# Kernel optimization log

Measured on AMD Instinct MI355X. Metric: run time of the kernel, lower is better.

## Reference

```python
import jax, jax.numpy as jnp
import numpy as np

ITEMNUM = 50000
NUM_HEADS = 4
EPS = 1e-8


def _ln(x, g, b):
    m = x.mean(-1, keepdims=True)
    v = ((x - m) ** 2).mean(-1, keepdims=True)
    return (x - m) * jax.lax.rsqrt(v + EPS) * g + b


def _forward(seqs_data, position, seqs, time_emb, pos_table, gate_W, gate_b,
             ln_attn_g, ln_attn_b, qW, qb, kW, kb, vW, vb,
             ln_ffn_g, ln_ffn_b, c1W, c1b, c2W, c2b, last_g, last_b):
    B, L, H = seqs.shape
    nb = qW.shape[0]
    hd = H // NUM_HEADS

    pe = pos_table[position]                      # [B,L,H]
    seqs = seqs + pe
    time = time_emb + pe
    # per-position per-block time gates, [B,L,nb]
    gates = jax.nn.sigmoid(jnp.einsum('blh,nh->bln', time, gate_W) + gate_b)

    keep = (seqs_data != ITEMNUM - 1)[..., None].astype(seqs.dtype)  # [B,L,1]
    seqs = seqs * keep
    tril = jnp.tril(jnp.ones((L, L), dtype=bool))  # causal: keep lower triangle
    neg_inf = jnp.asarray(-jnp.inf, seqs.dtype)
    scale = 1.0 / np.sqrt(hd).astype(np.float32)

    for i in range(nb):
        Q = _ln(seqs, ln_attn_g[i], ln_attn_b[i])
        q = Q @ qW[i].T + qb[i]
        k = time @ kW[i].T + kb[i]
        v = (seqs + time) @ vW[i].T + vb[i]
        # [B,nh,L,hd]
        q = q.reshape(B, L, NUM_HEADS, hd).transpose(0, 2, 1, 3)
        k = k.reshape(B, L, NUM_HEADS, hd).transpose(0, 2, 1, 3)
        v = v.reshape(B, L, NUM_HEADS, hd).transpose(0, 2, 1, 3)
        scores = jnp.einsum('bhqd,bhkd->bhqk', q, k) * scale  # [B,nh,L,L]
        tg = gates[:, :, i]                                   # [B,L]
        gate_mat = tg[:, None, :, None] * tg[:, None, None, :]  # [B,1,L,L] outer product
        scores = jnp.where(tril[None, None], scores * gate_mat, neg_inf)
        attn = jax.nn.softmax(scores, axis=-1)
        out = jnp.einsum('bhqk,bhkd->bhqd', attn, v)
        out = out.transpose(0, 2, 1, 3).reshape(B, L, H)
        x = Q + out
        x = _ln(x, ln_ffn_g[i], ln_ffn_b[i])
        # PointWiseFeedForward: two 1x1 convs == two linears, relu, residual
        h = jax.nn.relu(x @ c1W[i].T + c1b[i])
        seqs = (h @ c2W[i].T + c2b[i] + x) * keep

    return _ln(seqs, last_g, last_b)


def setup_inputs() -> dict:
    key = jax.random.key(0)
    B, L, H, NB, ML = 64, 512, 256, 2, 512
    ks = iter(jax.random.split(key, 32))
    nrm = lambda shape, s=0.05: jax.random.normal(next(ks), shape, jnp.float32) * s
    pos_table = nrm((ML, H), 0.02).at[0].set(0.0)  # padding_idx=0
    inp = {
        'seqs_data': jax.random.randint(next(ks), (B, L), 0, ITEMNUM - 1, jnp.int32),
        'seqs': nrm((B, L, H), 1.0),
        'position': jax.random.randint(next(ks), (B, L), 0, ML, jnp.int32),
        'time_emb': nrm((B, L, H), 1.0),
        'pos_table': pos_table,
        'gate_W': nrm((NB, H)), 'gate_b': jnp.zeros((NB,), jnp.float32),
        'ln_attn_g': jnp.ones((NB, H), jnp.float32), 'ln_attn_b': jnp.zeros((NB, H), jnp.float32),
        'qW': nrm((NB, H, H)), 'qb': jnp.zeros((NB, H), jnp.float32),
        'kW': nrm((NB, H, H)), 'kb': jnp.zeros((NB, H), jnp.float32),
        'vW': nrm((NB, H, H)), 'vb': jnp.zeros((NB, H), jnp.float32),
        'ln_ffn_g': jnp.ones((NB, H), jnp.float32), 'ln_ffn_b': jnp.zeros((NB, H), jnp.float32),
        'c1W': nrm((NB, H, H)), 'c1b': jnp.zeros((NB, H), jnp.float32),
        'c2W': nrm((NB, H, H)), 'c2b': jnp.zeros((NB, H), jnp.float32),
        'last_g': jnp.ones((H,), jnp.float32), 'last_b': jnp.zeros((H,), jnp.float32),
    }
    return inp


def reference(seqs_data, seqs, position, time_emb, pos_table, gate_W, gate_b,
              ln_attn_g, ln_attn_b, qW, qb, kW, kb, vW, vb,
              ln_ffn_g, ln_ffn_b, c1W, c1b, c2W, c2b, last_g, last_b):
    return _forward(seqs_data, position, seqs, time_emb, pos_table, gate_W, gate_b,
                    ln_attn_g, ln_attn_b, qW, qb, kW, kb, vW, vb,
                    ln_ffn_g, ln_ffn_b, c1W, c1b, c2W, c2b, last_g, last_b)
```

## Files before the change

kernel.cpp:

```cpp
#include <hip/hip_runtime.h>
#include <hip/hip_bf16.h>
#include <math.h>

#define NTOK 32768
#define Hdim 256
#define Ldim 512
#define Bdim 64
#define NHEAD 4
#define HD 64
#define PADV 49999

typedef __bf16 bf16x8 __attribute__((ext_vector_type(8)));
typedef __bf16 bf16x4 __attribute__((ext_vector_type(4)));
typedef float  f32x4  __attribute__((ext_vector_type(4)));
typedef unsigned short u16x8 __attribute__((ext_vector_type(8)));

union bf8u { bf16x8 v8; bf16x4 v4[2]; };

__device__ __forceinline__ unsigned short f2bf(float f) {
    unsigned int u = __float_as_uint(f);
    unsigned int r = (u + 0x7fffu + ((u >> 16) & 1u)) >> 16;
    return (unsigned short)r;
}
__device__ __forceinline__ float bf2f(unsigned short u) {
    return __uint_as_float(((unsigned int)u) << 16);
}

__device__ __forceinline__ void gload16(const void* g, void* l) {
    __builtin_amdgcn_global_load_lds((const __attribute__((address_space(1))) unsigned int*)g,
                                     (__attribute__((address_space(3))) unsigned int*)l,
                                     16, 0, 0);
}

__global__ __launch_bounds__(256)
void castw_kernel(const float* __restrict__ q, const float* __restrict__ k,
                  const float* __restrict__ v, const float* __restrict__ c1,
                  const float* __restrict__ c2, unsigned short* __restrict__ dst) {
    const float* srcs[5] = {q, k, v, c1, c2};
    const float* s = srcs[blockIdx.y];
    int idx = blockIdx.x * 1024 + threadIdx.x * 4;
    float4 f = *(const float4*)(s + idx);
    unsigned short* d = dst + (size_t)blockIdx.y * 131072 + idx;
    d[0] = f2bf(f.x); d[1] = f2bf(f.y); d[2] = f2bf(f.z); d[3] = f2bf(f.w);
}

__global__ __launch_bounds__(256)
void prep_ln_kernel(const int* __restrict__ seqs_data, const float* __restrict__ seqs,
                    const int* __restrict__ position, const float* __restrict__ time_emb,
                    const float* __restrict__ pos_table, const float* __restrict__ gate_W,
                    const float* __restrict__ gate_b,
                    const float* __restrict__ lnG, const float* __restrict__ lnB,
                    unsigned short* __restrict__ Tbf,
                    unsigned short* __restrict__ QXbf,
                    unsigned short* __restrict__ VINbf,
                    float* __restrict__ gates, float* __restrict__ keepv) {
    int tok  = blockIdx.x * 4 + (threadIdx.x >> 6);
    int lane = threadIdx.x & 63;
    size_t off = (size_t)tok * Hdim + lane * 4;
    int pos = position[tok];
    float4 pe = *(const float4*)(pos_table + (size_t)pos * Hdim + lane * 4);
    float4 sq = *(const float4*)(seqs + off);
    float4 tm = *(const float4*)(time_emb + off);
    float keep = (seqs_data[tok] != PADV) ? 1.0f : 0.0f;
    float4 t = {tm.x + pe.x, tm.y + pe.y, tm.z + pe.z, tm.w + pe.w};
    float4 s = {(sq.x + pe.x) * keep, (sq.y + pe.y) * keep,
                (sq.z + pe.z) * keep, (sq.w + pe.w) * keep};
    ushort4 tb = {f2bf(t.x), f2bf(t.y), f2bf(t.z), f2bf(t.w)};
    *(ushort4*)(Tbf + off) = tb;
    float4 gw0 = *(const float4*)(gate_W + lane * 4);
    float4 gw1 = *(const float4*)(gate_W + Hdim + lane * 4);
    float r0 = s.x + s.y + s.z + s.w;
    float r1 = s.x * s.x + s.y * s.y + s.z * s.z + s.w * s.w;
    float r2 = t.x * gw0.x + t.y * gw0.y + t.z * gw0.z + t.w * gw0.w;
    float r3 = t.x * gw1.x + t.y * gw1.y + t.z * gw1.z + t.w * gw1.w;
#pragma unroll
    for (int o = 1; o < 64; o <<= 1) {
        r0 += __shfl_xor(r0, o, 64);
        r1 += __shfl_xor(r1, o, 64);
        r2 += __shfl_xor(r2, o, 64);
        r3 += __shfl_xor(r3, o, 64);
    }
    float mean = r0 * (1.0f / Hdim);
    float var  = fmaxf(r1 * (1.0f / Hdim) - mean * mean, 0.0f);
    float rstd = rsqrtf(var + 1e-8f);
    if (lane == 0) {
        gates[(size_t)tok * 2 + 0] = 1.0f / (1.0f + __expf(-(r2 + gate_b[0])));
        gates[(size_t)tok * 2 + 1] = 1.0f / (1.0f + __expf(-(r3 + gate_b[1])));
        keepv[tok] = keep;
    }
    float4 g4 = *(const float4*)(lnG + lane * 4);
    float4 b4 = *(const float4*)(lnB + lane * 4);
    float4 y = {(s.x - mean) * rstd * g4.x + b4.x, (s.y - mean) * rstd * g4.y + b4.y,
                (s.z - mean) * rstd * g4.z + b4.z, (s.w - mean) * rstd * g4.w + b4.w};
    ushort4 yb = {f2bf(y.x), f2bf(y.y), f2bf(y.z), f2bf(y.w)};
    *(ushort4*)(QXbf + off) = yb;
    ushort4 vb = {f2bf(s.x + t.x), f2bf(s.y + t.y), f2bf(s.z + t.z), f2bf(s.w + t.w)};
    *(ushort4*)(VINbf + off) = vb;
}

#define GBM 128
#define GBN 128
#define GBK 64

__device__ __forceinline__ void stage64(const unsigned short* __restrict__ src,
                                        size_t rowBase, __bf16* lds, int tid, int kc) {
#pragma unroll
    for (int it = 0; it < 4; ++it) {
        int c = tid + it * 256;
        int r = c >> 3, sub = c & 7;
        int g = sub ^ (r & 7);
        gload16(src + (rowBase + r) * Hdim + kc + g * 8, lds + c * 8);
    }
}
__device__ __forceinline__ bf16x8 frag64(const __bf16* lds, int r, int g) {
    return *(const bf16x8*)(lds + r * 64 + (g ^ (r & 7)) * 8);
}

__global__ __launch_bounds__(256)
void gemm_qkv_kernel(const unsigned short* __restrict__ QXbf,
                     const unsigned short* __restrict__ Tbf,
                     const unsigned short* __restrict__ VINbf,
                     const unsigned short* __restrict__ qW,
                     const unsigned short* __restrict__ kW,
                     const unsigned short* __restrict__ vW,
                     const float* __restrict__ qb, const float* __restrict__ kb,
                     const float* __restrict__ vb,
                     unsigned short* __restrict__ Qbf,
                     unsigned short* __restrict__ Kbf,
                     unsigned short* __restrict__ VT) {
    __shared__ __align__(16) char smem[128 * 136 * 2];
    __bf16* As = (__bf16*)smem;
    __bf16* Ws = (__bf16*)(smem + 16384);
    __bf16 (*Ct)[136] = (__bf16 (*)[136])smem;
    int z = blockIdx.z;
    const unsigned short* A = (z == 0) ? QXbf : (z == 1) ? Tbf : VINbf;
    const unsigned short* W = (z == 0) ? qW : (z == 1) ? kW : vW;
    const float* bias       = (z == 0) ? qb : (z == 1) ? kb : vb;

    int tid = threadIdx.x, lane = tid & 63, w = tid >> 6;
    int wr = w >> 1, wc = w & 1;
    int m0 = blockIdx.y * GBM, n0 = blockIdx.x * GBN;
    f32x4 acc[4][4];
#pragma unroll
    for (int i = 0; i < 4; ++i)
#pragma unroll
        for (int j = 0; j < 4; ++j) acc[i][j] = (f32x4)(0.0f);
    int colq = lane & 15, kg = lane >> 4;
    for (int kc = 0; kc < Hdim; kc += GBK) {
        __syncthreads();
        stage64(A, m0, As, tid, kc);
        stage64(W, n0, Ws, tid, kc);
        __syncthreads();
        bf16x8 af[4][2], bfr[4][2];
#pragma unroll
        for (int i = 0; i < 4; ++i) {
            int r = wr * 64 + i * 16 + colq;
            af[i][0] = frag64(As, r, kg);
            af[i][1] = frag64(As, r, 4 + kg);
        }
#pragma unroll
        for (int j = 0; j < 4; ++j) {
            int r = wc * 64 + j * 16 + colq;
            bfr[j][0] = frag64(Ws, r, kg);
            bfr[j][1] = frag64(Ws, r, 4 + kg);
        }
#pragma unroll
        for (int i = 0; i < 4; ++i)
#pragma unroll
            for (int j = 0; j < 4; ++j) {
                acc[i][j] = __builtin_amdgcn_mfma_f32_16x16x32_bf16(af[i][0], bfr[j][0], acc[i][j], 0, 0, 0);
                acc[i][j] = __builtin_amdgcn_mfma_f32_16x16x32_bf16(af[i][1], bfr[j][1], acc[i][j], 0, 0, 0);
            }
    }
    int rowq = (lane >> 4) * 4;
    if (z < 2) {
        unsigned short* outBF = (z == 0) ? Qbf : Kbf;
#pragma unroll
        for (int i = 0; i < 4; ++i)
#pragma unroll
            for (int r = 0; r < 4; ++r) {
                int m = m0 + wr * 64 + i * 16 + rowq + r;
#pragma unroll
                for (int j = 0; j < 4; ++j) {
                    int n = n0 + wc * 64 + j * 16 + colq;
                    outBF[(size_t)m * Hdim + n] = f2bf(acc[i][j][r] + bias[n]);
                }
            }
    } else {
        __syncthreads();
#pragma unroll
        for (int i = 0; i < 4; ++i)
#pragma unroll
            for (int r = 0; r < 4; ++r) {
                int ml = wr * 64 + i * 16 + rowq + r;
#pragma unroll
                for (int j = 0; j < 4; ++j) {
                    int nl = wc * 64 + j * 16 + colq;
                    Ct[nl][ml] = (__bf16)(acc[i][j][r] + bias[n0 + nl]);
                }
            }
        __syncthreads();
        int bb = m0 >> 9, l0 = m0 & 511;
#pragma unroll
        for (int it = 0; it < 8; ++it) {
            int c = tid + it * 256;
            int nl = c >> 4;
            int o8 = (c & 15) * 8;
            int n = n0 + nl;
            int hh = n >> 6, dd = n & 63;
            bf16x8 v = *(const bf16x8*)&Ct[nl][o8];
            *(bf16x8*)(VT + ((((size_t)bb * NHEAD + hh) * HD + dd) * Ldim + l0 + o8)) = v;
        }
    }
}

#define FBM 64
#define FFN_LDS (32768 + 131072)

__device__ __forceinline__ int swz(int r, int g) {
    return (g & 24) | ((g & 7) ^ (r & 7));
}

__device__ __forceinline__ void ffn_stageW(const unsigned short* __restrict__ W,
                                           __bf16* Wst, int tid) {
#pragma unroll
    for (int it = 0; it < 32; ++it) {
        int c = tid + it * 256;
        int r = c >> 5, s = c & 31;
        int g = (s & 24) | ((s & 7) ^ (r & 7));
        gload16(W + (size_t)r * Hdim + g * 8, Wst + c * 8);
    }
}

__device__ __forceinline__ bf16x8 fragW(const __bf16* buf, int row, int slot8) {
    return *(const bf16x8*)(buf + row * 256 + swz(row, slot8) * 8);
}

__device__ __forceinline__ void ffn_gemm(const __bf16* Abuf, const __bf16* Wst,
                                         int w, int colq, int kg, f32x4 acc[4][4]) {
#pragma unroll
    for (int i = 0; i < 4; ++i)
#pragma unroll
        for (int j = 0; j < 4; ++j) acc[i][j] = (f32x4)(0.0f);
#pragma unroll
    for (int kc = 0; kc < Hdim; kc += 64) {
        bf16x8 af[4][2], bfr[4][2];
#pragma unroll
        for (int i = 0; i < 4; ++i) {
            int r = i * 16 + colq;
            af[i][0] = fragW(Abuf, r, (kc >> 3) + kg);
            af[i][1] = fragW(Abuf, r, (kc >> 3) + 4 + kg);
        }
#pragma unroll
        for (int j = 0; j < 4; ++j) {
            int n = w * 64 + j * 16 + colq;
            bfr[j][0] = fragW(Wst, n, (kc >> 3) + kg);
            bfr[j][1] = fragW(Wst, n, (kc >> 3) + 4 + kg);
        }
#pragma unroll
        for (int i = 0; i < 4; ++i)
#pragma unroll
            for (int j = 0; j < 4; ++j) {
                acc[i][j] = __builtin_amdgcn_mfma_f32_16x16x32_bf16(af[i][0], bfr[j][0], acc[i][j], 0, 0, 0);
                acc[i][j] = __builtin_amdgcn_mfma_f32_16x16x32_bf16(af[i][1], bfr[j][1], acc[i][j], 0, 0, 0);
            }
    }
}

__global__ __launch_bounds__(256)
void ffn_kernel(const unsigned short* __restrict__ Qx,
                const unsigned short* __restrict__ Qa,
                const float* __restrict__ lnG, const float* __restrict__ lnB,
                const unsigned short* __restrict__ c1Wb, const float* __restrict__ c1b,
                const unsigned short* __restrict__ c2Wb, const float* __restrict__ c2b,
                const float* __restrict__ keepv,
                const unsigned short* __restrict__ Tbf,
                const float* __restrict__ oG, const float* __restrict__ oB,
                float* __restrict__ outF,
                unsigned short* __restrict__ QxOut,
                unsigned short* __restrict__ VINout) {
    extern __shared__ __align__(16) char smem[];
    __bf16* Abuf = (__bf16*)smem;
    __bf16* Wst  = (__bf16*)(smem + 32768);

    int m0  = blockIdx.x * FBM;
    int tid = threadIdx.x, lane = tid & 63, w = tid >> 6;
    int colq = lane & 15, kg = lane >> 4;
    int rowq = kg * 4;

    ffn_stageW(c1Wb, Wst, tid);

    u16x8 qvr[8], avr[8];
#pragma unroll
    for (int it = 0; it < 8; ++it) {
        int c = tid + it * 256;
        int r = c >> 5, g = c & 31;
        size_t off = (size_t)(m0 + r) * Hdim + g * 8;
        qvr[it] = *(const u16x8*)(Qx + off);
        avr[it] = *(const u16x8*)(Qa + off);
    }
    u16x8 xnreg[8];
#pragma unroll
    for (int it = 0; it < 8; ++it) {
        int c = tid + it * 256;
        int r = c >> 5, g = c & 31, col = g * 8;
        float x[8];
        float cs = 0.0f, cq = 0.0f;
#pragma unroll
        for (int j = 0; j < 8; ++j) {
            x[j] = bf2f(qvr[it][j]) + bf2f(avr[it][j]);
            cs += x[j]; cq += x[j] * x[j];
        }
#pragma unroll
        for (int o = 1; o < 32; o <<= 1) {
            cs += __shfl_xor(cs, o, 32);
            cq += __shfl_xor(cq, o, 32);
        }
        float mean = cs * (1.0f / Hdim);
        float var  = fmaxf(cq * (1.0f / Hdim) - mean * mean, 0.0f);
        float rstd = rsqrtf(var + 1e-8f);
        float4 g0 = *(const float4*)(lnG + col), g1 = *(const float4*)(lnG + col + 4);
        float4 b0 = *(const float4*)(lnB + col), b1 = *(const float4*)(lnB + col + 4);
        float gv[8] = {g0.x, g0.y, g0.z, g0.w, g1.x, g1.y, g1.z, g1.w};
        float bv[8] = {b0.x, b0.y, b0.z, b0.w, b1.x, b1.y, b1.z, b1.w};
        u16x8 xn;
#pragma unroll
        for (int j = 0; j < 8; ++j)
            xn[j] = f2bf((x[j] - mean) * rstd * gv[j] + bv[j]);
        xnreg[it] = xn;
        *(u16x8*)(Abuf + r * 256 + swz(r, g) * 8) = xn;
    }
    __syncthreads();

    f32x4 acc[4][4];
    ffn_gemm(Abuf, Wst, w, colq, kg, acc);
    __syncthreads();
    ffn_stageW(c2Wb, Wst, tid);
    float bj[4];
#pragma unroll
    for (int j = 0; j < 4; ++j) bj[j] = c1b[w * 64 + j * 16 + colq];
#pragma unroll
    for (int i = 0; i < 4; ++i)
#pragma unroll
        for (int r = 0; r < 4; ++r) {
            int m = i * 16 + rowq + r;
#pragma unroll
            for (int j = 0; j < 4; ++j) {
                int n = w * 64 + j * 16 + colq;
                float v = fmaxf(acc[i][j][r] + bj[j], 0.0f);
                Abuf[m * 256 + swz(m, n >> 3) * 8 + (n & 7)] = (__bf16)v;
            }
        }
    __syncthreads();

    ffn_gemm(Abuf, Wst, w, colq, kg, acc);
    __syncthreads();
#pragma unroll
    for (int j = 0; j < 4; ++j) bj[j] = c2b[w * 64 + j * 16 + colq];
#pragma unroll
    for (int i = 0; i < 4; ++i)
#pragma unroll
        for (int r = 0; r < 4; ++r) {
            int m = i * 16 + rowq + r;
#pragma unroll
            for (int j = 0; j < 4; ++j) {
                int n = w * 64 + j * 16 + colq;
                Abuf[m * 256 + swz(m, n >> 3) * 8 + (n & 7)] = (__bf16)(acc[i][j][r] + bj[j]);
            }
        }
    __syncthreads();

    u16x8 zvr[8];
#pragma unroll
    for (int it = 0; it < 8; ++it) {
        int c = tid + it * 256;
        int r = c >> 5, g = c & 31;
        zvr[it] = *(const u16x8*)(Abuf + r * 256 + swz(r, g) * 8);
    }
#pragma unroll
    for (int it = 0; it < 8; ++it) {
        int c = tid + it * 256;
        int r = c >> 5, g = c & 31, col = g * 8;
        float kf = keepv[m0 + r];
        float sv[8];
        float cs = 0.0f, cq = 0.0f;
#pragma unroll
        for (int j = 0; j < 8; ++j) {
            sv[j] = (bf2f(zvr[it][j]) + bf2f(xnreg[it][j])) * kf;
            cs += sv[j]; cq += sv[j] * sv[j];
        }
#pragma unroll
        for (int o = 1; o < 32; o <<= 1) {
            cs += __shfl_xor(cs, o, 32);
            cq += __shfl_xor(cq, o, 32);
        }
        float mean = cs * (1.0f / Hdim);
        float var  = fmaxf(cq * (1.0f / Hdim) - mean * mean, 0.0f);
        float rstd = rsqrtf(var + 1e-8f);
        float4 g0 = *(const float4*)(oG + col), g1 = *(const float4*)(oG + col + 4);
        float4 b0 = *(const float4*)(oB + col), b1 = *(const float4*)(oB + col + 4);
        float gv[8] = {g0.x, g0.y, g0.z, g0.w, g1.x, g1.y, g1.z, g1.w};
        float bv[8] = {b0.x, b0.y, b0.z, b0.w, b1.x, b1.y, b1.z, b1.w};
        size_t off = (size_t)(m0 + r) * Hdim + col;
        float y[8];
#pragma unroll
        for (int j = 0; j < 8; ++j)
            y[j] = (sv[j] - mean) * rstd * gv[j] + bv[j];
        if (outF) {
            float4 o0 = {y[0], y[1], y[2], y[3]};
            float4 o1 = {y[4], y[5], y[6], y[7]};
            *(float4*)(outF + off)     = o0;
            *(float4*)(outF + off + 4) = o1;
        } else {
            u16x8 yb, vb;
            u16x8 tv = *(const u16x8*)(Tbf + off);
#pragma unroll
            for (int j = 0; j < 8; ++j) {
                yb[j] = f2bf(y[j]);
                vb[j] = f2bf(sv[j] + bf2f(tv[j]));
            }
            *(u16x8*)(QxOut + off)  = yb;
            *(u16x8*)(VINout + off) = vb;
        }
    }
}

#define AKS 68
#define AVS 516
#define APS 68
#define ATTN_LDS (512 * AKS * 2 + 64 * AVS * 2 + 192 * APS * 2)
__global__ __launch_bounds__(768, 1)
void attn_mfma_kernel(const unsigned short* __restrict__ Qg,
                      const unsigned short* __restrict__ Kg,
                      const unsigned short* __restrict__ VTg,
                      const float* __restrict__ gates,
                      unsigned short* __restrict__ Ob, int blk) {
    extern __shared__ __align__(16) char smem[];
    __bf16 (*Ks)[AKS]  = (__bf16 (*)[AKS])smem;
    __bf16 (*VTs)[AVS] = (__bf16 (*)[AVS])(smem + 512 * AKS * 2);
    __bf16 (*Ps)[APS]  = (__bf16 (*)[APS])(smem + 512 * AKS * 2 + 64 * AVS * 2);
    int h = blockIdx.x & 3, b = blockIdx.x >> 2;
    int tid = threadIdx.x, lane = tid & 63, w = tid >> 6;
    int colq = lane & 15, grp = lane >> 4;
    int rowq = grp * 4, kq = grp * 8;

    size_t baseK = (size_t)b * Ldim * Hdim + h * HD;
    for (int c = tid; c < 4096; c += 768) {
        int r = c >> 3, o = (c & 7) * 8;
        bf8u u;
        u.v8 = *(const bf16x8*)(Kg + baseK + (size_t)r * Hdim + o);
        *(bf16x4*)&Ks[r][o]     = u.v4[0];
        *(bf16x4*)&Ks[r][o + 4] = u.v4[1];
    }
    size_t baseV = ((size_t)b * NHEAD + h) * HD * Ldim;
    for (int c = tid; c < 4096; c += 768) {
        int d = c >> 6, k = (c & 63) * 8;
        bf8u u;
        u.v8 = *(const bf16x8*)(VTg + baseV + (size_t)d * Ldim + k);
        *(bf16x4*)&VTs[d][k]     = u.v4[0];
        *(bf16x4*)&VTs[d][k + 4] = u.v4[1];
    }
    __syncthreads();

    const float lscale = 0.125f * 1.44269504f;
    int gl[3], ng;
    if (w < 4)      { gl[0] = w;     gl[1] = 8 + w;  gl[2] = 28 + w; ng = 3; }
    else if (w < 8) { gl[0] = w;     gl[1] = 8 + w;  gl[2] = 16 + w; ng = 3; }
    else            { gl[0] = 8 + w; gl[1] = 16 + w; gl[2] = 0;      ng = 2; }

    for (int gi = 0; gi < ng; ++gi) {
        int g = gl[gi];
        int q0 = g * 16;
        size_t qrow = (size_t)(b * Ldim + q0 + colq) * Hdim + h * HD;
        bf16x8 afq0 = *(const bf16x8*)(Qg + qrow + kq);
        bf16x8 afq1 = *(const bf16x8*)(Qg + qrow + 32 + kq);
        float gql[4];
#pragma unroll
        for (int r = 0; r < 4; ++r)
            gql[r] = gates[((size_t)b * Ldim + q0 + rowq + r) * 2 + blk] * lscale;

        float lrun[4] = {0.0f, 0.0f, 0.0f, 0.0f};
        f32x4 accO[4];
#pragma unroll
        for (int jd = 0; jd < 4; ++jd) accO[jd] = (f32x4)(0.0f);

        int nfull = g >> 2;
        for (int kt = 0; kt <= nfull; ++kt) {
            int k0 = kt * 64;
            bool diag = (kt == nfull);
            f32x4 sv[4];
#pragma unroll
            for (int j = 0; j < 4; ++j) sv[j] = (f32x4)(0.0f);
#pragma unroll
            for (int j = 0; j < 4; ++j) {
                int kr = k0 + j * 16 + colq;
                bf8u b0, b1;
                b0.v4[0] = *(const bf16x4*)&Ks[kr][kq];
                b0.v4[1] = *(const bf16x4*)&Ks[kr][kq + 4];
                b1.v4[0] = *(const bf16x4*)&Ks[kr][32 + kq];
                b1.v4[1] = *(const bf16x4*)&Ks[kr][32 + kq + 4];
                sv[j] = __builtin_amdgcn_mfma_f32_16x16x32_bf16(afq0, b0.v8, sv[j], 0, 0, 0);
                sv[j] = __builtin_amdgcn_mfma_f32_16x16x32_bf16(afq1, b1.v8, sv[j], 0, 0, 0);
            }
            float gkv[4];
#pragma unroll
            for (int j = 0; j < 4; ++j)
                gkv[j] = gates[((size_t)b * Ldim + k0 + j * 16 + colq) * 2 + blk];
#pragma unroll
            for (int r = 0; r < 4; ++r) {
                float su = 0.0f;
                float p4[4];
                if (diag) {
                    int qg = q0 + rowq + r;
#pragma unroll
                    for (int j = 0; j < 4; ++j) {
                        float v = sv[j][r] * gql[r] * gkv[j];
                        v = (k0 + j * 16 + colq > qg) ? -1e38f : v;
                        float e = exp2f(v);
                        p4[j] = e;
                        su += e;
                    }
                } else {
#pragma unroll
                    for (int j = 0; j < 4; ++j) {
                        float e = exp2f(sv[j][r] * gql[r] * gkv[j]);
                        p4[j] = e;
                        su += e;
                    }
                }
#pragma unroll
                for (int off = 1; off < 16; off <<= 1)
                    su += __shfl_xor(su, off, 16);
                lrun[r] += su;
#pragma unroll
                for (int j = 0; j < 4; ++j)
                    Ps[w * 16 + rowq + r][j * 16 + colq] = (__bf16)p4[j];
            }
            bf8u a0, a1;
            a0.v4[0] = *(const bf16x4*)&Ps[w * 16 + colq][kq];
            a0.v4[1] = *(const bf16x4*)&Ps[w * 16 + colq][kq + 4];
            a1.v4[0] = *(const bf16x4*)&Ps[w * 16 + colq][32 + kq];
            a1.v4[1] = *(const bf16x4*)&Ps[w * 16 + colq][32 + kq + 4];
#pragma unroll
            for (int jd = 0; jd < 4; ++jd) {
                int vr = jd * 16 + colq;
                bf8u v0, v1;
                v0.v4[0] = *(const bf16x4*)&VTs[vr][k0 + kq];
                v0.v4[1] = *(const bf16x4*)&VTs[vr][k0 + kq + 4];
                v1.v4[0] = *(const bf16x4*)&VTs[vr][k0 + 32 + kq];
                v1.v4[1] = *(const bf16x4*)&VTs[vr][k0 + 32 + kq + 4];
                accO[jd] = __builtin_amdgcn_mfma_f32_16x16x32_bf16(a0.v8, v0.v8, accO[jd], 0, 0, 0);
                accO[jd] = __builtin_amdgcn_mfma_f32_16x16x32_bf16(a1.v8, v1.v8, accO[jd], 0, 0, 0);
            }
        }
#pragma unroll
        for (int r = 0; r < 4; ++r) {
            float inv = 1.0f / lrun[r];
#pragma unroll
            for (int jd = 0; jd < 4; ++jd)
                Ob[(size_t)(b * Ldim + q0 + rowq + r) * Hdim + h * HD + jd * 16 + colq] =
                    f2bf(accO[jd][r] * inv);
        }
    }
}

extern "C" void kernel_launch(void* const* d_in, const int* in_sizes, int n_in,
                              void* d_out, int out_size, void* d_ws, size_t ws_size,
                              hipStream_t stream) {
    const int*   seqs_data = (const int*)d_in[0];
    const float* seqs      = (const float*)d_in[1];
    const int*   position  = (const int*)d_in[2];
    const float* time_emb  = (const float*)d_in[3];
    const float* pos_table = (const float*)d_in[4];
    const float* gate_W    = (const float*)d_in[5];
    const float* gate_b    = (const float*)d_in[6];
    const float* ln_attn_g = (const float*)d_in[7];
    const float* ln_attn_b = (const float*)d_in[8];
    const float* qW        = (const float*)d_in[9];
    const float* qb        = (const float*)d_in[10];
    const float* kW        = (const float*)d_in[11];
    const float* kb        = (const float*)d_in[12];
    const float* vW        = (const float*)d_in[13];
    const float* vb        = (const float*)d_in[14];
    const float* ln_ffn_g  = (const float*)d_in[15];
    const float* ln_ffn_b  = (const float*)d_in[16];
    const float* c1W       = (const float*)d_in[17];
    const float* c1b       = (const float*)d_in[18];
    const float* c2W       = (const float*)d_in[19];
    const float* c2b       = (const float*)d_in[20];
    const float* last_g    = (const float*)d_in[21];
    const float* last_b    = (const float*)d_in[22];

    size_t BUF = (size_t)NTOK * Hdim;
    float* fws = (float*)d_ws;
    float* GATES = fws;
    float* KEEP  = GATES + (size_t)NTOK * 2;
    unsigned short* bws   = (unsigned short*)(KEEP + NTOK);
    unsigned short* Tbf   = bws;
    unsigned short* QXbf  = Tbf + BUF;
    unsigned short* VINbf = QXbf + BUF;
    unsigned short* HIDbf = VINbf + BUF;
    unsigned short* Qbf   = HIDbf + BUF;
    unsigned short* Kbf   = Qbf + BUF;
    unsigned short* VTbf  = Kbf + BUF;
    unsigned short* QAbf  = VTbf + BUF;
    unsigned short* Zbf   = QAbf + BUF;
    unsigned short* Wbf   = Zbf + BUF;
    size_t WB = (size_t)Hdim * Hdim;
    unsigned short* qWbf  = Wbf;
    unsigned short* kWbf  = Wbf + 2 * WB;
    unsigned short* vWbf  = Wbf + 4 * WB;
    unsigned short* c1Wbf = Wbf + 6 * WB;
    unsigned short* c2Wbf = Wbf + 8 * WB;

    castw_kernel<<<dim3(128, 5), 256, 0, stream>>>(qW, kW, vW, c1W, c2W, Wbf);
    prep_ln_kernel<<<NTOK / 4, 256, 0, stream>>>(seqs_data, seqs, position, time_emb,
                                                 pos_table, gate_W, gate_b,
                                                 ln_attn_g, ln_attn_b,
                                                 Tbf, QXbf, VINbf, GATES, KEEP);

    dim3 qkvgrid(Hdim / GBN, NTOK / GBM, 3);
    for (int i = 0; i < 2; ++i) {
        gemm_qkv_kernel<<<qkvgrid, 256, 0, stream>>>(QXbf, Tbf, VINbf,
                                                     qWbf + i * WB, kWbf + i * WB, vWbf + i * WB,
                                                     qb + i * Hdim, kb + i * Hdim, vb + i * Hdim,
                                                     Qbf, Kbf, VTbf);
        attn_mfma_kernel<<<Bdim * NHEAD, 768, ATTN_LDS, stream>>>(Qbf, Kbf, VTbf, GATES, QAbf, i);
        ffn_kernel<<<NTOK / FBM, 256, FFN_LDS, stream>>>(
            QXbf, QAbf,
            ln_ffn_g + i * Hdim, ln_ffn_b + i * Hdim,
            c1Wbf + i * WB, c1b + i * Hdim,
            c2Wbf + i * WB, c2b + i * Hdim,
            KEEP, Tbf,
            (i == 0) ? ln_attn_g + Hdim : last_g,
            (i == 0) ? ln_attn_b + Hdim : last_b,
            (i == 0) ? nullptr : (float*)d_out,
            QXbf, VINbf);
    }
}
```

Before: 367.7 us.

## Double-buffer FFN weight K-slices with 128-row tiles and 512 threads; boost attention MFMA priority

The FFN kernel now processes 128 tokens per block with 8 waves in a 2x4 layout. Instead of staging a full 256x256 weight matrix in LDS, it streams 64-wide K slices into two alternating buffers, prefetching the next slice while computing the current one. This cuts LDS per block and overlaps weight loads with MFMA work, and each staged weight tile is reused across more rows. The attention kernel also raises wave priority around its MFMA sections. The risk is extra barriers per K step and only one block per CU under launch bounds (512,1).

New measurement: 341.4 us. 1.08x faster.

```diff
diff --git a/kernel.cpp b/kernel.cpp
--- a/kernel.cpp
+++ b/kernel.cpp
@@ -214,48 +214,49 @@
     }
 }
 
-#define FBM 64
-#define FFN_LDS (32768 + 131072)
+#define FBM 128
+#define FFN_LDS (65536 + 32768 * 2)
 
 __device__ __forceinline__ int swz(int r, int g) {
     return (g & 24) | ((g & 7) ^ (r & 7));
 }
 
-__device__ __forceinline__ void ffn_stageW(const unsigned short* __restrict__ W,
+__device__ __forceinline__ void ffn_stageK(const unsigned short* __restrict__ W, int kc,
                                            __bf16* Wst, int tid) {
 #pragma unroll
-    for (int it = 0; it < 32; ++it) {
-        int c = tid + it * 256;
-        int r = c >> 5, s = c & 31;
-        int g = (s & 24) | ((s & 7) ^ (r & 7));
-        gload16(W + (size_t)r * Hdim + g * 8, Wst + c * 8);
-    }
-}
-
-__device__ __forceinline__ bf16x8 fragW(const __bf16* buf, int row, int slot8) {
-    return *(const bf16x8*)(buf + row * 256 + swz(row, slot8) * 8);
-}
-
-__device__ __forceinline__ void ffn_gemm(const __bf16* Abuf, const __bf16* Wst,
-                                         int w, int colq, int kg, f32x4 acc[4][4]) {
+    for (int it = 0; it < 4; ++it) {
+        int c = tid + it * 512;
+        int r = c >> 3, sub = c & 7;
+        int g = sub ^ (r & 7);
+        gload16(W + (size_t)r * Hdim + kc + g * 8, Wst + c * 8);
+    }
+}
+
+__device__ __forceinline__ void ffn_gemm(const unsigned short* __restrict__ W,
+                                         const __bf16* Abuf, __bf16* Wst0, __bf16* Wst1,
+                                         int tid, int wr, int wc, int colq, int kg,
+                                         f32x4 acc[4][4]) {
 #pragma unroll
     for (int i = 0; i < 4; ++i)
 #pragma unroll
         for (int j = 0; j < 4; ++j) acc[i][j] = (f32x4)(0.0f);
 #pragma unroll
-    for (int kc = 0; kc < Hdim; kc += 64) {
+    for (int kc = 0; kc < Hdim; kc += GBK) {
+        const __bf16* cur = ((kc >> 6) & 1) ? Wst1 : Wst0;
+        __bf16*       nxt = ((kc >> 6) & 1) ? Wst0 : Wst1;
+        if (kc + GBK < Hdim) ffn_stageK(W, kc + GBK, nxt, tid);
         bf16x8 af[4][2], bfr[4][2];
 #pragma unroll
         for (int i = 0; i < 4; ++i) {
-            int r = i * 16 + colq;
-            af[i][0] = fragW(Abuf, r, (kc >> 3) + kg);
-            af[i][1] = fragW(Abuf, r, (kc >> 3) + 4 + kg);
+            int r = wr * 64 + i * 16 + colq;
+            af[i][0] = *(const bf16x8*)(Abuf + r * 256 + ((kc >> 3) | (kg ^ (r & 7))) * 8);
+            af[i][1] = *(const bf16x8*)(Abuf + r * 256 + ((kc >> 3) | ((4 + kg) ^ (r & 7))) * 8);
         }
 #pragma unroll
         for (int j = 0; j < 4; ++j) {
-            int n = w * 64 + j * 16 + colq;
-            bfr[j][0] = fragW(Wst, n, (kc >> 3) + kg);
-            bfr[j][1] = fragW(Wst, n, (kc >> 3) + 4 + kg);
+            int n = wc * 64 + j * 16 + colq;
+            bfr[j][0] = frag64(cur, n, kg);
+            bfr[j][1] = frag64(cur, n, 4 + kg);
         }
 #pragma unroll
         for (int i = 0; i < 4; ++i)
@@ -264,10 +265,13 @@
                 acc[i][j] = __builtin_amdgcn_mfma_f32_16x16x32_bf16(af[i][0], bfr[j][0], acc[i][j], 0, 0, 0);
                 acc[i][j] = __builtin_amdgcn_mfma_f32_16x16x32_bf16(af[i][1], bfr[j][1], acc[i][j], 0, 0, 0);
             }
-    }
-}
-
-__global__ __launch_bounds__(256)
+        asm volatile("s_waitcnt vmcnt(0)" ::: "memory");
+        __builtin_amdgcn_s_barrier();
+        asm volatile("" ::: "memory");
+    }
+}
+
+__global__ __launch_bounds__(512, 1)
 void ffn_kernel(const unsigned short* __restrict__ Qx,
                 const unsigned short* __restrict__ Qa,
                 const float* __restrict__ lnG, const float* __restrict__ lnB,
@@ -281,19 +285,21 @@
                 unsigned short* __restrict__ VINout) {
     extern __shared__ __align__(16) char smem[];
     __bf16* Abuf = (__bf16*)smem;
-    __bf16* Wst  = (__bf16*)(smem + 32768);
+    __bf16* Wst0 = (__bf16*)(smem + 65536);
+    __bf16* Wst1 = (__bf16*)(smem + 65536 + 32768);
 
     int m0  = blockIdx.x * FBM;
     int tid = threadIdx.x, lane = tid & 63, w = tid >> 6;
+    int wr = w >> 2, wc = w & 3;
     int colq = lane & 15, kg = lane >> 4;
     int rowq = kg * 4;
 
-    ffn_stageW(c1Wb, Wst, tid);
+    ffn_stageK(c1Wb, 0, Wst0, tid);
 
     u16x8 qvr[8], avr[8];
 #pragma unroll
     for (int it = 0; it < 8; ++it) {
-        int c = tid + it * 256;
+        int c = tid + it * 512;
         int r = c >> 5, g = c & 31;
         size_t off = (size_t)(m0 + r) * Hdim + g * 8;
         qvr[it] = *(const u16x8*)(Qx + off);
@@ -302,7 +308,7 @@
     u16x8 xnreg[8];
 #pragma unroll
     for (int it = 0; it < 8; ++it) {
-        int c = tid + it * 256;
+        int c = tid + it * 512;
         int r = c >> 5, g = c & 31, col = g * 8;
         float x[8];
         float cs = 0.0f, cq = 0.0f;
@@ -333,53 +339,51 @@
     __syncthreads();
 
     f32x4 acc[4][4];
-    ffn_gemm(Abuf, Wst, w, colq, kg, acc);
-    __syncthreads();
-    ffn_stageW(c2Wb, Wst, tid);
+    ffn_gemm(c1Wb, Abuf, Wst0, Wst1, tid, wr, wc, colq, kg, acc);
+    ffn_stageK(c2Wb, 0, Wst0, tid);
     float bj[4];
 #pragma unroll
-    for (int j = 0; j < 4; ++j) bj[j] = c1b[w * 64 + j * 16 + colq];
+    for (int j = 0; j < 4; ++j) bj[j] = c1b[wc * 64 + j * 16 + colq];
 #pragma unroll
     for (int i = 0; i < 4; ++i)
 #pragma unroll
         for (int r = 0; r < 4; ++r) {
-            int m = i * 16 + rowq + r;
+            int m = wr * 64 + i * 16 + rowq + r;
 #pragma unroll
             for (int j = 0; j < 4; ++j) {
-                int n = w * 64 + j * 16 + colq;
+                int n = wc * 64 + j * 16 + colq;
                 float v = fmaxf(acc[i][j][r] + bj[j], 0.0f);
                 Abuf[m * 256 + swz(m, n >> 3) * 8 + (n & 7)] = (__bf16)v;
             }
         }
     __syncthreads();
 
-    ffn_gemm(Abuf, Wst, w, colq, kg, acc);
+    ffn_gemm(c2Wb, Abuf, Wst0, Wst1, tid, wr, wc, colq, kg, acc);
+#pragma unroll
+    for (int j = 0; j < 4; ++j) bj[j] = c2b[wc * 64 + j * 16 + colq];
+#pragma unroll
+    for (int i = 0; i < 4; ++i)
+#pragma unroll
+        for (int r = 0; r < 4; ++r) {
+            int m = wr * 64 + i * 16 + rowq + r;
+#pragma unroll
+            for (int j = 0; j < 4; ++j) {
+                int n = wc * 64 + j * 16 + colq;
+                Abuf[m * 256 + swz(m, n >> 3) * 8 + (n & 7)] = (__bf16)(acc[i][j][r] + bj[j]);
+            }
+        }
     __syncthreads();
-#pragma unroll
-    for (int j = 0; j < 4; ++j) bj[j] = c2b[w * 64 + j * 16 + colq];
-#pragma unroll
-    for (int i = 0; i < 4; ++i)
-#pragma unroll
-        for (int r = 0; r < 4; ++r) {
-            int m = i * 16 + rowq + r;
-#pragma unroll
-            for (int j = 0; j < 4; ++j) {
-                int n = w * 64 + j * 16 + colq;
-                Abuf[m * 256 + swz(m, n >> 3) * 8 + (n & 7)] = (__bf16)(acc[i][j][r] + bj[j]);
-            }
-        }
-    __syncthreads();
 
     u16x8 zvr[8];
 #pragma unroll
     for (int it = 0; it < 8; ++it) {
-        int c = tid + it * 256;
+        int c = tid + it * 512;
         int r = c >> 5, g = c & 31;
         zvr[it] = *(const u16x8*)(Abuf + r * 256 + swz(r, g) * 8);
     }
 #pragma unroll
     for (int it = 0; it < 8; ++it) {
-        int c = tid + it * 256;
+        int c = tid + it * 512;
         int r = c >> 5, g = c & 31, col = g * 8;
         float kf = keepv[m0 + r];
         float sv[8];
@@ -491,6 +495,7 @@
             f32x4 sv[4];
 #pragma unroll
             for (int j = 0; j < 4; ++j) sv[j] = (f32x4)(0.0f);
+            __builtin_amdgcn_s_setprio(1);
 #pragma unroll
             for (int j = 0; j < 4; ++j) {
                 int kr = k0 + j * 16 + colq;
@@ -502,6 +507,7 @@
                 sv[j] = __builtin_amdgcn_mfma_f32_16x16x32_bf16(afq0, b0.v8, sv[j], 0, 0, 0);
                 sv[j] = __builtin_amdgcn_mfma_f32_16x16x32_bf16(afq1, b1.v8, sv[j], 0, 0, 0);
             }
+            __builtin_amdgcn_s_setprio(0);
             float gkv[4];
 #pragma unroll
             for (int j = 0; j < 4; ++j)
@@ -541,6 +547,7 @@
             a0.v4[1] = *(const bf16x4*)&Ps[w * 16 + colq][kq + 4];
             a1.v4[0] = *(const bf16x4*)&Ps[w * 16 + colq][32 + kq];
             a1.v4[1] = *(const bf16x4*)&Ps[w * 16 + colq][32 + kq + 4];
+            __builtin_amdgcn_s_setprio(1);
 #pragma unroll
             for (int jd = 0; jd < 4; ++jd) {
                 int vr = jd * 16 + colq;
@@ -552,6 +559,7 @@
                 accO[jd] = __builtin_amdgcn_mfma_f32_16x16x32_bf16(a0.v8, v0.v8, accO[jd], 0, 0, 0);
                 accO[jd] = __builtin_amdgcn_mfma_f32_16x16x32_bf16(a1.v8, v1.v8, accO[jd], 0, 0, 0);
             }
+            __builtin_amdgcn_s_setprio(0);
         }
 #pragma unroll
         for (int r = 0; r < 4; ++r) {
@@ -626,7 +634,7 @@
                                                      qb + i * Hdim, kb + i * Hdim, vb + i * Hdim,
                                                      Qbf, Kbf, VTbf);
         attn_mfma_kernel<<<Bdim * NHEAD, 768, ATTN_LDS, stream>>>(Qbf, Kbf, VTbf, GATES, QAbf, i);
-        ffn_kernel<<<NTOK / FBM, 256, FFN_LDS, stream>>>(
+        ffn_kernel<<<NTOK / FBM, 512, FFN_LDS, stream>>>(
             QXbf, QAbf,
             ln_ffn_g + i * Hdim, ln_ffn_b + i * Hdim,
             c1Wbf + i * WB, c1b + i * Hdim,
```
